# Optimization experiments

Measured on AMD Instinct MI355X. Metric: run time of the kernel, lower is better.

The kernel has to match this reference:

```python
import jax, jax.numpy as jnp
import numpy as np

B, T, IN, OUT, NGROUPS = 1, 64, 4096, 8192, 16


def setup_inputs() -> dict:
    key = jax.random.key(0)
    k1, k2, k3, k4 = jax.random.split(key, 4)
    x = jax.random.normal(k1, (B, T, IN), dtype=jnp.float32)
    qweight = jax.random.randint(k2, (OUT, IN), 0, 256, dtype=jnp.int32)
    # qrange plays the role of (max-min)/255 per group: small positive scale
    qrange = jax.random.uniform(k3, (OUT, NGROUPS), dtype=jnp.float32) * 0.01
    qmin = jax.random.normal(k4, (OUT, NGROUPS), dtype=jnp.float32) * 0.1
    return {"x": x, "qweight": qweight, "qrange": qrange, "qmin": qmin}


def reference(x, qweight, qrange, qmin):
    # qweight: [O, I] uint8-valued codes, 16 quant groups along the input dim.
    O, I = qweight.shape
    gs = I // NGROUPS  # group size along input dim
    # Dequantize per group: w = q * range[group] + min[group]
    q = qweight.astype(jnp.float32).reshape(O, NGROUPS, gs)
    w = q * qrange[:, :, None] + qmin[:, :, None]  # [O, 16, gs]
    w = w.reshape(O, I)
    # out[b,t,o] = sum_i x[b,t,i] * w[o,i]
    return jnp.einsum("bti,oi->bto", x, w)
```

## Files before the change

### kernel.cpp

```cpp
#include <hip/hip_runtime.h>
#include <stdint.h>

#define T_DIM 64
#define IN_DIM 4096
#define OUT_DIM 8192
#define NGROUPS 16
#define GS 256
#define SPLITK 8
#define KCHUNK (IN_DIM / SPLITK)
#define BK 64
#define NSTAGES (KCHUNK / BK)
#define NTILE 256
#define WCOLS 32
#define OUT_ELEMS (T_DIM * OUT_DIM)
#define PART_OFF (1u << 20)

typedef __attribute__((ext_vector_type(4))) float f32x4;
typedef __attribute__((ext_vector_type(8))) __bf16 bf16x8;

__global__ void zero_kernel(float4* __restrict__ p, int n4) {
    int i = blockIdx.x * blockDim.x + threadIdx.x;
    if (i < n4) p[i] = make_float4(0.f, 0.f, 0.f, 0.f);
}

__global__ void cvt_kernel(const float* __restrict__ x, __bf16* __restrict__ xb, int n) {
    int i = (blockIdx.x * blockDim.x + threadIdx.x) * 8;
    if (i < n) {
        float4 f0 = *(const float4*)(x + i);
        float4 f1 = *(const float4*)(x + i + 4);
        bf16x8 o;
        o[0] = (__bf16)f0.x; o[1] = (__bf16)f0.y; o[2] = (__bf16)f0.z; o[3] = (__bf16)f0.w;
        o[4] = (__bf16)f1.x; o[5] = (__bf16)f1.y; o[6] = (__bf16)f1.z; o[7] = (__bf16)f1.w;
        *(bf16x8*)(xb + i) = o;
    }
}

__global__ void reduce_kernel(const float4* __restrict__ part, float4* __restrict__ out, int n4) {
    int i = blockIdx.x * blockDim.x + threadIdx.x;
    if (i < n4) {
        float4 s = part[i];
        #pragma unroll
        for (int k = 1; k < SPLITK; ++k) {
            float4 v = part[i + k * n4];
            s.x += v.x; s.y += v.y; s.z += v.z; s.w += v.w;
        }
        out[i] = s;
    }
}

__device__ __forceinline__ void gld_lds16(const int* g, int* l) {
    __builtin_amdgcn_global_load_lds(
        (const __attribute__((address_space(1))) void*)g,
        (__attribute__((address_space(3))) void*)l, 16, 0, 0);
}

template<bool PART>
__global__ __launch_bounds__(512, 2)
void qgemm(const float* __restrict__ x, const __bf16* __restrict__ xb,
           const int* __restrict__ qw, const float* __restrict__ qrange,
           const float* __restrict__ qmin, float* __restrict__ out)
{
    __shared__ int lds[2][NTILE][BK];

    const int lane  = threadIdx.x & 63;
    const int wv    = threadIdx.x >> 6;
    const int r     = lane & 15;
    const int q4    = lane >> 4;
    const int obase = blockIdx.x * NTILE;
    const int ks    = blockIdx.y;
    const int kbase = ks * KCHUNK;
    const int rl0   = wv * WCOLS + r;
    const int o0    = obase + rl0;
    const int o1    = o0 + 16;

    float sc[2][2], mi[2][2];
    #pragma unroll
    for (int g = 0; g < 2; ++g) {
        sc[0][g] = qrange[o0 * NGROUPS + ks * 2 + g];
        mi[0][g] = qmin[o0 * NGROUPS + ks * 2 + g];
        sc[1][g] = qrange[o1 * NGROUPS + ks * 2 + g];
        mi[1][g] = qmin[o1 * NGROUPS + ks * 2 + g];
    }

    const __bf16* xrow = xb + (size_t)r * IN_DIM + kbase + q4 * 8;

    f32x4 acc[4][2] = {};
    bf16x8 xf[2][4][2];

    auto stage_w = [&](int s, int b) {
        #pragma unroll
        for (int i = 0; i < 8; ++i) {
            const int rl = wv * WCOLS + i * 4 + (lane >> 4);
            const int c  = (lane & 15) ^ (rl & 7);
            const int* gp = qw + (size_t)(obase + rl) * IN_DIM + kbase + s * BK + c * 4;
            gld_lds16(gp, &lds[b][wv * WCOLS + i * 4][0]);
        }
    };

    auto xload = [&](int s, int buf) {
        #pragma unroll
        for (int m = 0; m < 4; ++m) {
            #pragma unroll
            for (int kk = 0; kk < 2; ++kk) {
                const int koff = s * BK + kk * 32;
                xf[buf][m][kk] = *(const bf16x8*)(xrow + (size_t)(m * 16) * IN_DIM + koff);
            }
        }
    };

    auto compute = [&](int s, int b, int xbuf) {
        const int g = s >> 2;
        #pragma unroll
        for (int kk = 0; kk < 2; ++kk) {
            bf16x8 bfr[2];
            #pragma unroll
            for (int n = 0; n < 2; ++n) {
                const int rl = rl0 + n * 16;
                const int t  = q4 * 2;
                const int p0 = kk * 8 + ((t    ) ^ (rl & 7));
                const int p1 = kk * 8 + ((t + 1) ^ (rl & 7));
                int4 c0 = *(const int4*)&lds[b][rl][p0 * 4];
                int4 c1 = *(const int4*)&lds[b][rl][p1 * 4];
                const float s0 = sc[n][g], m0 = mi[n][g];
                bfr[n][0] = (__bf16)((float)c0.x * s0 + m0);
                bfr[n][1] = (__bf16)((float)c0.y * s0 + m0);
                bfr[n][2] = (__bf16)((float)c0.z * s0 + m0);
                bfr[n][3] = (__bf16)((float)c0.w * s0 + m0);
                bfr[n][4] = (__bf16)((float)c1.x * s0 + m0);
                bfr[n][5] = (__bf16)((float)c1.y * s0 + m0);
                bfr[n][6] = (__bf16)((float)c1.z * s0 + m0);
                bfr[n][7] = (__bf16)((float)c1.w * s0 + m0);
            }
            #pragma unroll
            for (int m = 0; m < 4; ++m) {
                acc[m][0] = __builtin_amdgcn_mfma_f32_16x16x32_bf16(xf[xbuf][m][kk], bfr[0], acc[m][0], 0, 0, 0);
                acc[m][1] = __builtin_amdgcn_mfma_f32_16x16x32_bf16(xf[xbuf][m][kk], bfr[1], acc[m][1], 0, 0, 0);
            }
        }
    };

    stage_w(0, 0);
    xload(0, 0);
    #pragma unroll
    for (int s = 0; s < NSTAGES; ++s) {
        if (s + 1 < NSTAGES) {
            stage_w(s + 1, (s + 1) & 1);
            xload(s + 1, (s + 1) & 1);
            asm volatile("s_waitcnt vmcnt(16)" ::: "memory");
        } else {
            asm volatile("s_waitcnt vmcnt(0)" ::: "memory");
        }
        __builtin_amdgcn_sched_barrier(0);
        compute(s, s & 1, s & 1);
    }

    if constexpr (PART) {
        float* part = out + (size_t)ks * OUT_ELEMS;
        #pragma unroll
        for (int m = 0; m < 4; ++m) {
            #pragma unroll
            for (int j = 0; j < 4; ++j) {
                const int t = m * 16 + q4 * 4 + j;
                part[(size_t)t * OUT_DIM + o0] = acc[m][0][j];
                part[(size_t)t * OUT_DIM + o1] = acc[m][1][j];
            }
        }
    } else {
        #pragma unroll
        for (int m = 0; m < 4; ++m) {
            #pragma unroll
            for (int j = 0; j < 4; ++j) {
                const int t = m * 16 + q4 * 4 + j;
                unsafeAtomicAdd(&out[(size_t)t * OUT_DIM + o0], acc[m][0][j]);
                unsafeAtomicAdd(&out[(size_t)t * OUT_DIM + o1], acc[m][1][j]);
            }
        }
    }
}

extern "C" void kernel_launch(void* const* d_in, const int* in_sizes, int n_in,
                              void* d_out, int out_size, void* d_ws, size_t ws_size,
                              hipStream_t stream)
{
    const float* x      = (const float*)d_in[0];
    const int*   qw     = (const int*)d_in[1];
    const float* qrange = (const float*)d_in[2];
    const float* qmin   = (const float*)d_in[3];
    float* out = (float*)d_out;

    const int nx = T_DIM * IN_DIM;
    const size_t xb_bytes = (size_t)nx * sizeof(unsigned short);
    const size_t part_bytes = (size_t)SPLITK * OUT_ELEMS * sizeof(float);

    if (ws_size >= PART_OFF + part_bytes && ws_size >= xb_bytes) {
        __bf16* xbp  = (__bf16*)d_ws;
        float*  part = (float*)((char*)d_ws + PART_OFF);
        cvt_kernel<<<dim3(nx / 8 / 256), dim3(256), 0, stream>>>(x, xbp, nx);
        qgemm<true><<<dim3(OUT_DIM / NTILE, SPLITK), dim3(512), 0, stream>>>(x, xbp, qw, qrange, qmin, part);
        const int n4 = OUT_ELEMS / 4;
        reduce_kernel<<<dim3(n4 / 256), dim3(256), 0, stream>>>((const float4*)part, (float4*)out, n4);
    } else {
        const int n4 = out_size / 4;
        zero_kernel<<<dim3((n4 + 255) / 256), dim3(256), 0, stream>>>((float4*)d_out, n4);
        __bf16* xbp = (__bf16*)d_ws;
        cvt_kernel<<<dim3(nx / 8 / 256), dim3(256), 0, stream>>>(x, xbp, nx);
        qgemm<false><<<dim3(OUT_DIM / NTILE, SPLITK), dim3(512), 0, stream>>>(x, xbp, qw, qrange, qmin, out);
    }
}
```

Baseline: 40.34 us.

## Halve N tile per block and store split-K partials in bf16

Shrinks the output tile from 256 to 128 columns so each wave computes 16 columns. This doubles the grid to 512 blocks and allows 4 blocks per CU via launch bounds, targeting better occupancy and load balance. Split-K partial sums are now written and read as bf16 instead of fp32, which halves partial-buffer traffic in the GEMM epilogue and the reduce kernel. The cost is lower precision in the partials, and x fragments are reloaded per narrower tile, so there is less reuse of x.

```diff
diff --git a/kernel.cpp b/kernel.cpp
--- a/kernel.cpp
+++ b/kernel.cpp
@@ -10,8 +10,8 @@
 #define KCHUNK (IN_DIM / SPLITK)
 #define BK 64
 #define NSTAGES (KCHUNK / BK)
-#define NTILE 256
-#define WCOLS 32
+#define NTILE 128
+#define WCOLS 16
 #define OUT_ELEMS (T_DIM * OUT_DIM)
 #define PART_OFF (1u << 20)
 
@@ -35,16 +35,20 @@
     }
 }
 
-__global__ void reduce_kernel(const float4* __restrict__ part, float4* __restrict__ out, int n4) {
+__global__ void reduce_kernel(const __bf16* __restrict__ part, float* __restrict__ out, int n8) {
     int i = blockIdx.x * blockDim.x + threadIdx.x;
-    if (i < n4) {
-        float4 s = part[i];
-        #pragma unroll
-        for (int k = 1; k < SPLITK; ++k) {
-            float4 v = part[i + k * n4];
-            s.x += v.x; s.y += v.y; s.z += v.z; s.w += v.w;
-        }
-        out[i] = s;
+    if (i < n8) {
+        float s[8] = {};
+        #pragma unroll
+        for (int k = 0; k < SPLITK; ++k) {
+            bf16x8 v = *(const bf16x8*)(part + (size_t)k * OUT_ELEMS + (size_t)i * 8);
+            #pragma unroll
+            for (int j = 0; j < 8; ++j) s[j] += (float)v[j];
+        }
+        float4 o0 = make_float4(s[0], s[1], s[2], s[3]);
+        float4 o1 = make_float4(s[4], s[5], s[6], s[7]);
+        *(float4*)(out + (size_t)i * 8)     = o0;
+        *(float4*)(out + (size_t)i * 8 + 4) = o1;
     }
 }
 
@@ -55,10 +59,11 @@
 }
 
 template<bool PART>
-__global__ __launch_bounds__(512, 2)
+__global__ __launch_bounds__(512, 4)
 void qgemm(const float* __restrict__ x, const __bf16* __restrict__ xb,
            const int* __restrict__ qw, const float* __restrict__ qrange,
-           const float* __restrict__ qmin, float* __restrict__ out)
+           const float* __restrict__ qmin, float* __restrict__ out,
+           __bf16* __restrict__ bpart)
 {
     __shared__ int lds[2][NTILE][BK];
 
@@ -71,25 +76,22 @@
     const int kbase = ks * KCHUNK;
     const int rl0   = wv * WCOLS + r;
     const int o0    = obase + rl0;
-    const int o1    = o0 + 16;
-
-    float sc[2][2], mi[2][2];
+
+    float sc[2], mi[2];
     #pragma unroll
     for (int g = 0; g < 2; ++g) {
-        sc[0][g] = qrange[o0 * NGROUPS + ks * 2 + g];
-        mi[0][g] = qmin[o0 * NGROUPS + ks * 2 + g];
-        sc[1][g] = qrange[o1 * NGROUPS + ks * 2 + g];
-        mi[1][g] = qmin[o1 * NGROUPS + ks * 2 + g];
+        sc[g] = qrange[o0 * NGROUPS + ks * 2 + g];
+        mi[g] = qmin[o0 * NGROUPS + ks * 2 + g];
     }
 
     const __bf16* xrow = xb + (size_t)r * IN_DIM + kbase + q4 * 8;
 
-    f32x4 acc[4][2] = {};
+    f32x4 acc[4] = {};
     bf16x8 xf[2][4][2];
 
     auto stage_w = [&](int s, int b) {
         #pragma unroll
-        for (int i = 0; i < 8; ++i) {
+        for (int i = 0; i < 4; ++i) {
             const int rl = wv * WCOLS + i * 4 + (lane >> 4);
             const int c  = (lane & 15) ^ (rl & 7);
             const int* gp = qw + (size_t)(obase + rl) * IN_DIM + kbase + s * BK + c * 4;
@@ -110,32 +112,26 @@
 
     auto compute = [&](int s, int b, int xbuf) {
         const int g = s >> 2;
+        const float s0 = sc[g], m0 = mi[g];
         #pragma unroll
         for (int kk = 0; kk < 2; ++kk) {
-            bf16x8 bfr[2];
-            #pragma unroll
-            for (int n = 0; n < 2; ++n) {
-                const int rl = rl0 + n * 16;
-                const int t  = q4 * 2;
-                const int p0 = kk * 8 + ((t    ) ^ (rl & 7));
-                const int p1 = kk * 8 + ((t + 1) ^ (rl & 7));
-                int4 c0 = *(const int4*)&lds[b][rl][p0 * 4];
-                int4 c1 = *(const int4*)&lds[b][rl][p1 * 4];
-                const float s0 = sc[n][g], m0 = mi[n][g];
-                bfr[n][0] = (__bf16)((float)c0.x * s0 + m0);
-                bfr[n][1] = (__bf16)((float)c0.y * s0 + m0);
-                bfr[n][2] = (__bf16)((float)c0.z * s0 + m0);
-                bfr[n][3] = (__bf16)((float)c0.w * s0 + m0);
-                bfr[n][4] = (__bf16)((float)c1.x * s0 + m0);
-                bfr[n][5] = (__bf16)((float)c1.y * s0 + m0);
-                bfr[n][6] = (__bf16)((float)c1.z * s0 + m0);
-                bfr[n][7] = (__bf16)((float)c1.w * s0 + m0);
-            }
-            #pragma unroll
-            for (int m = 0; m < 4; ++m) {
-                acc[m][0] = __builtin_amdgcn_mfma_f32_16x16x32_bf16(xf[xbuf][m][kk], bfr[0], acc[m][0], 0, 0, 0);
-                acc[m][1] = __builtin_amdgcn_mfma_f32_16x16x32_bf16(xf[xbuf][m][kk], bfr[1], acc[m][1], 0, 0, 0);
-            }
+            const int t  = q4 * 2;
+            const int p0 = kk * 8 + ((t    ) ^ (rl0 & 7));
+            const int p1 = kk * 8 + ((t + 1) ^ (rl0 & 7));
+            int4 c0 = *(const int4*)&lds[b][rl0][p0 * 4];
+            int4 c1 = *(const int4*)&lds[b][rl0][p1 * 4];
+            bf16x8 bfr;
+            bfr[0] = (__bf16)((float)c0.x * s0 + m0);
+            bfr[1] = (__bf16)((float)c0.y * s0 + m0);
+            bfr[2] = (__bf16)((float)c0.z * s0 + m0);
+            bfr[3] = (__bf16)((float)c0.w * s0 + m0);
+            bfr[4] = (__bf16)((float)c1.x * s0 + m0);
+            bfr[5] = (__bf16)((float)c1.y * s0 + m0);
+            bfr[6] = (__bf16)((float)c1.z * s0 + m0);
+            bfr[7] = (__bf16)((float)c1.w * s0 + m0);
+            #pragma unroll
+            for (int m = 0; m < 4; ++m)
+                acc[m] = __builtin_amdgcn_mfma_f32_16x16x32_bf16(xf[xbuf][m][kk], bfr, acc[m], 0, 0, 0);
         }
     };
 
@@ -146,7 +142,7 @@
         if (s + 1 < NSTAGES) {
             stage_w(s + 1, (s + 1) & 1);
             xload(s + 1, (s + 1) & 1);
-            asm volatile("s_waitcnt vmcnt(16)" ::: "memory");
+            asm volatile("s_waitcnt vmcnt(12)" ::: "memory");
         } else {
             asm volatile("s_waitcnt vmcnt(0)" ::: "memory");
         }
@@ -155,14 +151,13 @@
     }
 
     if constexpr (PART) {
-        float* part = out + (size_t)ks * OUT_ELEMS;
+        __bf16* part = bpart + (size_t)ks * OUT_ELEMS;
         #pragma unroll
         for (int m = 0; m < 4; ++m) {
             #pragma unroll
             for (int j = 0; j < 4; ++j) {
                 const int t = m * 16 + q4 * 4 + j;
-                part[(size_t)t * OUT_DIM + o0] = acc[m][0][j];
-                part[(size_t)t * OUT_DIM + o1] = acc[m][1][j];
+                part[(size_t)t * OUT_DIM + o0] = (__bf16)acc[m][j];
             }
         }
     } else {
@@ -171,8 +166,7 @@
             #pragma unroll
             for (int j = 0; j < 4; ++j) {
                 const int t = m * 16 + q4 * 4 + j;
-                unsafeAtomicAdd(&out[(size_t)t * OUT_DIM + o0], acc[m][0][j]);
-                unsafeAtomicAdd(&out[(size_t)t * OUT_DIM + o1], acc[m][1][j]);
+                unsafeAtomicAdd(&out[(size_t)t * OUT_DIM + o0], acc[m][j]);
             }
         }
     }
@@ -189,21 +183,23 @@
     float* out = (float*)d_out;
 
     const int nx = T_DIM * IN_DIM;
-    const size_t xb_bytes = (size_t)nx * sizeof(unsigned short);
-    const size_t part_bytes = (size_t)SPLITK * OUT_ELEMS * sizeof(float);
+    const size_t xb_bytes   = (size_t)nx * sizeof(unsigned short);
+    const size_t part_bytes = (size_t)SPLITK * OUT_ELEMS * sizeof(short);
 
     if (ws_size >= PART_OFF + part_bytes && ws_size >= xb_bytes) {
         __bf16* xbp  = (__bf16*)d_ws;
-        float*  part = (float*)((char*)d_ws + PART_OFF);
+        __bf16* part = (__bf16*)((char*)d_ws + PART_OFF);
         cvt_kernel<<<dim3(nx / 8 / 256), dim3(256), 0, stream>>>(x, xbp, nx);
-        qgemm<true><<<dim3(OUT_DIM / NTILE, SPLITK), dim3(512), 0, stream>>>(x, xbp, qw, qrange, qmin, part);
-        const int n4 = OUT_ELEMS / 4;
-        reduce_kernel<<<dim3(n4 / 256), dim3(256), 0, stream>>>((const float4*)part, (float4*)out, n4);
+        qgemm<true><<<dim3(OUT_DIM / NTILE, SPLITK), dim3(512), 0, stream>>>(
+            x, xbp, qw, qrange, qmin, out, part);
+        const int n8 = OUT_ELEMS / 8;
+        reduce_kernel<<<dim3(n8 / 256), dim3(256), 0, stream>>>(part, out, n8);
     } else {
         const int n4 = out_size / 4;
         zero_kernel<<<dim3((n4 + 255) / 256), dim3(256), 0, stream>>>((float4*)d_out, n4);
         __bf16* xbp = (__bf16*)d_ws;
         cvt_kernel<<<dim3(nx / 8 / 256), dim3(256), 0, stream>>>(x, xbp, nx);
-        qgemm<false><<<dim3(OUT_DIM / NTILE, SPLITK), dim3(512), 0, stream>>>(x, xbp, qw, qrange, qmin, out);
-    }
-}
+        qgemm<false><<<dim3(OUT_DIM / NTILE, SPLITK), dim3(512), 0, stream>>>(
+            x, xbp, qw, qrange, qmin, out, nullptr);
+    }
+}
```

Result: slower. 49.21 us (+22.0%).
